# Kernel tuning notes

Measured on AMD Instinct MI355X. Metric: run time of the kernel, lower is better.

Reference implementation:

```python
import jax, jax.numpy as jnp
import numpy as np

N_HEAD = 16
MAX_SEQ_LEN = 2048
RATIO = 1
NEG_INF = -jnp.inf


def make_alibi_bias(n_head: int, max_seq_len: int, ratio: int) -> jnp.ndarray:
    # bias[t, s] = s*ratio - t, masked to -inf where > 0 (future positions)
    s = jnp.arange(max_seq_len)[None, :] * ratio            # [1, S]
    t = jnp.arange(max_seq_len * ratio)[:, None]            # [T, 1]
    bias = (s - t).astype(jnp.float32)                      # [T, S]
    bias = jnp.where(bias > 0, NEG_INF, bias)
    # per-head slopes: cumprod of 2^(-8/n_head) -> m_i = 2^(-8*(i+1)/n_head)
    m = jnp.cumprod(jnp.full((n_head,), 2.0 ** (-8.0 / n_head), dtype=jnp.float32))
    return bias[None, :, :] * m[:, None, None]              # [H, T, S]


def setup_inputs() -> dict:
    key = jax.random.key(0)
    kq, kk, kv = jax.random.split(key, 3)
    B, T, D = 2, 2048, 1024
    return {
        "q": jax.random.normal(kq, (B, T, D), dtype=jnp.float32),
        "k": jax.random.normal(kk, (B, T, D), dtype=jnp.float32),
        "v": jax.random.normal(kv, (B, T, D), dtype=jnp.float32),
    }


def reference(q, k, v):
    B, T, D = q.shape
    S = k.shape[1]
    H = N_HEAD
    dh = D // H
    # split heads: [B, T, D] -> [B, H, T, dh]
    qh = q.reshape(B, T, H, dh).transpose(0, 2, 1, 3)
    kh = k.reshape(B, S, H, dh).transpose(0, 2, 1, 3)
    vh = v.reshape(B, S, H, dh).transpose(0, 2, 1, 3)

    scores = jnp.einsum("bhtd,bhsd->bhts", qh, kh) / jnp.sqrt(jnp.float32(dh))
    bias = make_alibi_bias(H, MAX_SEQ_LEN, RATIO)[:, -T:, -S:]  # [H, T, S]
    attn = jax.nn.softmax(scores + bias[None], axis=-1)
    out = jnp.einsum("bhts,bhsd->bhtd", attn, vh)
    # gather heads: [B, H, T, dh] -> [B, T, D]
    return out.transpose(0, 2, 1, 3).reshape(B, T, D)
```

## Files before the change

### kernel.cpp

```cpp
#include <hip/hip_runtime.h>

#define N_HEAD 16
#define DHEAD 64
#define TSEQ 2048
#define DMODEL 1024
#define BATCH 2

typedef __bf16 bf16x8 __attribute__((ext_vector_type(8)));
typedef float f32x4 __attribute__((ext_vector_type(4)));

union BF8 { bf16x8 v; uint4 u; unsigned short us[8]; };

#if __has_builtin(__builtin_amdgcn_exp2f)
#define EXP2F(x) __builtin_amdgcn_exp2f(x)
#else
#define EXP2F(x) exp2f(x)
#endif

__device__ __forceinline__ void gload_lds16(const void* g, void* l) {
    __builtin_amdgcn_global_load_lds(
        (const __attribute__((address_space(1))) void*)g,
        (__attribute__((address_space(3))) void*)l, 16, 0, 0);
}

__device__ __forceinline__ unsigned short f2bf(float f) {
    unsigned u = __float_as_uint(f);
    u += 0x7fffu + ((u >> 16) & 1u);
    return (unsigned short)(u >> 16);
}

__device__ __forceinline__ bf16x8 load_bf8_f32(const float* p) {
    const float4 f0 = *(const float4*)p;
    const float4 f1 = *(const float4*)(p + 4);
    BF8 r;
    r.us[0] = f2bf(f0.x); r.us[1] = f2bf(f0.y);
    r.us[2] = f2bf(f0.z); r.us[3] = f2bf(f0.w);
    r.us[4] = f2bf(f1.x); r.us[5] = f2bf(f1.y);
    r.us[6] = f2bf(f1.z); r.us[7] = f2bf(f1.w);
    return r.v;
}

__global__ __launch_bounds__(256) void prep(const float* __restrict__ K,
                                            const float* __restrict__ V,
                                            unsigned short* __restrict__ Kp,
                                            unsigned short* __restrict__ Vt)
{
    __shared__ float tl[64][65];
    const int bh = blockIdx.y, b = bh >> 4, h = bh & 15;
    const int s0 = blockIdx.x * 64;
    const int t = threadIdx.x;
    const int r16 = t >> 4, c4 = (t & 15) * 4;
    #pragma unroll
    for (int pass = 0; pass < 4; ++pass) {
        const int row = pass * 16 + r16;
        const size_t goff = ((size_t)(b * TSEQ + s0 + row)) * DMODEL + h * DHEAD + c4;
        const float4 fk = *(const float4*)(K + goff);
        ushort4 ok;
        ok.x = f2bf(fk.x); ok.y = f2bf(fk.y); ok.z = f2bf(fk.z); ok.w = f2bf(fk.w);
        *(ushort4*)(Kp + (((size_t)bh * TSEQ + s0 + row) << 6) + c4) = ok;
        const float4 fv = *(const float4*)(V + goff);
        tl[row][c4 + 0] = fv.x; tl[row][c4 + 1] = fv.y;
        tl[row][c4 + 2] = fv.z; tl[row][c4 + 3] = fv.w;
    }
    __syncthreads();
    const int d = t >> 2, sc = (t & 3) * 16;
    union { unsigned short us[8]; uint4 u; } pk0, pk1;
    #pragma unroll
    for (int j = 0; j < 8; ++j) pk0.us[j] = f2bf(tl[sc + j][d]);
    #pragma unroll
    for (int j = 0; j < 8; ++j) pk1.us[j] = f2bf(tl[sc + 8 + j][d]);
    unsigned short* vo = Vt + ((size_t)bh * DHEAD + d) * TSEQ + s0 + sc;
    *(uint4*)vo = pk0.u;
    *(uint4*)(vo + 8) = pk1.u;
}

__global__ __launch_bounds__(256, 2) void alibi_attn(
    const float* __restrict__ Q, const unsigned short* __restrict__ Kp,
    const unsigned short* __restrict__ Vt, float* __restrict__ O)
{
    __shared__ __align__(16) unsigned short kbuf[2][4096];
    __shared__ __align__(16) unsigned short vbuf[2][4096];
    __shared__ __align__(16) unsigned short p_lds[4][32][72];

    const int wave = threadIdx.x >> 6;
    const int lane = threadIdx.x & 63;
    const int quad = lane >> 4;
    const int l16  = lane & 15;

    const int bh = blockIdx.x;
    const int b  = bh >> 4, h = bh & 15;
    const int sy = blockIdx.y;
    const int sx = (sy < 8) ? (15 - sy) : (sy - 8);

    const float LOG2E   = 1.44269504088896f;
    const float slope   = exp2f(-0.5f * (float)(h + 1));
    const float bslope2 = slope * LOG2E;
    const float sscale2 = 0.125f * LOG2E;
    const float step64  = 64.0f * bslope2;

    const float*    qp  = Q + (size_t)b * TSEQ * DMODEL + (size_t)h * DHEAD;
    const char*     kpb = (const char*)(Kp + (size_t)bh * TSEQ * DHEAD);
    const char*     vpb = (const char*)(Vt + (size_t)bh * DHEAD * TSEQ);

    const int base_w = sx * 128 + wave * 32;
    const int amax_w = (base_w + 31) >> 6;
    const int amax_b = 2 * sx + 1;

    const int st_r = lane >> 3;
    const int st_c = (lane & 7) ^ st_r;
    const int j0 = wave * 2;
    const int kg_off0 = (j0 * 8 + st_r) * 128 + st_c * 16;
    const int kg_off1 = kg_off0 + 8 * 128;
    const int vg_off0 = (j0 * 8 + st_r) * 4096 + st_c * 16;
    const int vg_off1 = vg_off0 + 8 * 4096;
    const int lds_o0 = j0 * 1024, lds_o1 = j0 * 1024 + 1024;

    auto stage = [&](int t) {
        const char* kg = kpb + (size_t)t * 8192;
        const char* vg = vpb + (size_t)t * 128;
        char* kd = (char*)kbuf[t & 1];
        char* vd = (char*)vbuf[t & 1];
        gload_lds16(kg + kg_off0, kd + lds_o0);
        gload_lds16(kg + kg_off1, kd + lds_o1);
        gload_lds16(vg + vg_off0, vd + lds_o0);
        gload_lds16(vg + vg_off1, vd + lds_o1);
    };

    const int koff0 = l16 * 128 + (((0 * 4 + quad) ^ (l16 & 7)) * 16);
    const int koff1 = l16 * 128 + (((1 * 4 + quad) ^ (l16 & 7)) * 16);

    stage(0);

    bf16x8 aq[2][2];
    #pragma unroll
    for (int qs = 0; qs < 2; ++qs) {
        const float* qr = qp + (size_t)(base_w + qs * 16 + l16) * DMODEL + quad * 8;
        aq[qs][0] = load_bf8_f32(qr);
        aq[qs][1] = load_bf8_f32(qr + 32);
    }

    const f32x4 zero4 = {0.f, 0.f, 0.f, 0.f};
    f32x4 o[2][4], lp[2];
    float dbq[2][4];
    #pragma unroll
    for (int qs = 0; qs < 2; ++qs) {
        lp[qs] = zero4;
        #pragma unroll
        for (int nt = 0; nt < 4; ++nt) {
            o[qs][nt] = zero4;
            dbq[qs][nt] = (float)(nt * 16 + l16 - (base_w + qs * 16 + quad * 4)) * bslope2;
        }
    }

    __syncthreads();

    for (int t = 0; t <= amax_b; ++t) {
        if (t < amax_b) stage(t + 1);

        if (t <= amax_w) {
            const char* kb = (const char*)kbuf[t & 1];
            const char* vb = (const char*)vbuf[t & 1];

            f32x4 s[2][4];
            #pragma unroll
            for (int nt = 0; nt < 4; ++nt) {
                BF8 k0, k1;
                k0.u = *(const uint4*)(kb + koff0 + nt * 2048);
                k1.u = *(const uint4*)(kb + koff1 + nt * 2048);
                #pragma unroll
                for (int qs = 0; qs < 2; ++qs) {
                    f32x4 acc = zero4;
                    acc = __builtin_amdgcn_mfma_f32_16x16x32_bf16(aq[qs][0], k0.v, acc, 0, 0, 0);
                    acc = __builtin_amdgcn_mfma_f32_16x16x32_bf16(aq[qs][1], k1.v, acc, 0, 0, 0);
                    s[qs][nt] = acc;
                }
            }
            uint4 vf[4][2];
            #pragma unroll
            for (int nt = 0; nt < 4; ++nt) {
                vf[nt][0] = *(const uint4*)(vb + koff0 + nt * 2048);
                vf[nt][1] = *(const uint4*)(vb + koff1 + nt * 2048);
            }

            const bool masked = (t == amax_w);
            const int kv0 = t * 64;
            #pragma unroll
            for (int qs = 0; qs < 2; ++qs)
                #pragma unroll
                for (int nt = 0; nt < 4; ++nt) {
                    f32x4 p;
                    #pragma unroll
                    for (int r = 0; r < 4; ++r)
                        p[r] = EXP2F(fmaf(s[qs][nt][r], sscale2,
                                          dbq[qs][nt] - (float)r * bslope2));
                    if (masked) {
                        const int di = kv0 + nt * 16 + l16 - (base_w + qs * 16 + quad * 4);
                        #pragma unroll
                        for (int r = 0; r < 4; ++r)
                            if (di - r > 0) p[r] = 0.f;
                    }
                    lp[qs] += p;
                    #pragma unroll
                    for (int r = 0; r < 4; ++r)
                        p_lds[wave][qs * 16 + quad * 4 + r][nt * 16 + l16] =
                            (unsigned short)(__float_as_uint(p[r]) >> 16);
                    dbq[qs][nt] += step64;
                }

            asm volatile("s_waitcnt lgkmcnt(0)" ::: "memory");
            BF8 pa[2][2];
            #pragma unroll
            for (int qs = 0; qs < 2; ++qs) {
                pa[qs][0].u = *(const uint4*)&p_lds[wave][qs * 16 + l16][quad * 8];
                pa[qs][1].u = *(const uint4*)&p_lds[wave][qs * 16 + l16][32 + quad * 8];
            }
            #pragma unroll
            for (int qs = 0; qs < 2; ++qs)
                #pragma unroll
                for (int nt = 0; nt < 4; ++nt) {
                    BF8 v0, v1;
                    v0.u = vf[nt][0];
                    v1.u = vf[nt][1];
                    o[qs][nt] = __builtin_amdgcn_mfma_f32_16x16x32_bf16(pa[qs][0].v, v0.v, o[qs][nt], 0, 0, 0);
                    o[qs][nt] = __builtin_amdgcn_mfma_f32_16x16x32_bf16(pa[qs][1].v, v1.v, o[qs][nt], 0, 0, 0);
                }
        }
        __syncthreads();
    }

    #pragma unroll
    for (int qs = 0; qs < 2; ++qs) {
        float ls[4];
        #pragma unroll
        for (int r = 0; r < 4; ++r) {
            float v = lp[qs][r];
            v += __shfl_xor(v, 1);
            v += __shfl_xor(v, 2);
            v += __shfl_xor(v, 4);
            v += __shfl_xor(v, 8);
            ls[r] = v;
        }
        #pragma unroll
        for (int nt = 0; nt < 4; ++nt)
            #pragma unroll
            for (int r = 0; r < 4; ++r) {
                const int trow = base_w + qs * 16 + quad * 4 + r;
                O[((size_t)b * TSEQ + trow) * DMODEL + h * DHEAD + nt * 16 + l16] =
                    o[qs][nt][r] / ls[r];
            }
    }
}

extern "C" void kernel_launch(void* const* d_in, const int* in_sizes, int n_in,
                              void* d_out, int out_size, void* d_ws, size_t ws_size,
                              hipStream_t stream) {
    const float* q = (const float*)d_in[0];
    const float* k = (const float*)d_in[1];
    const float* v = (const float*)d_in[2];
    float* out = (float*)d_out;

    unsigned short* Kp = (unsigned short*)d_ws;
    unsigned short* Vt = Kp + (size_t)BATCH * N_HEAD * TSEQ * DHEAD;

    prep<<<dim3(TSEQ / 64, BATCH * N_HEAD), 256, 0, stream>>>(k, v, Kp, Vt);
    alibi_attn<<<dim3(BATCH * N_HEAD, 16), 256, 0, stream>>>(q, Kp, Vt, out);
}
```

Baseline: 143.3 us.

## Switch attention to fp16 with transposed S so P feeds PV MFMA from registers

Converts K/V/Q staging from bf16 to fp16 using packed round-toward-zero conversion. Computes the score tile transposed (K as the A operand) so the exp'd probabilities land in registers in the layout the 16x16x16 f16 MFMA B/A operand expects, which removes the per-wave P round-trip through LDS and its wait. Blocks shrink to 128 threads covering 64 query rows with a 32-way grid, which removes the per-wave idle iterations of the old 128-row causal blocks. The costs are more, smaller MFMAs for PV, fp16 range risk for unnormalised probabilities, and less K/V reuse per block.

New measurement: 135.1 us. -5.8%, faster.

```diff
diff --git a/kernel.cpp b/kernel.cpp
--- a/kernel.cpp
+++ b/kernel.cpp
@@ -6,10 +6,14 @@
 #define DMODEL 1024
 #define BATCH 2
 
-typedef __bf16 bf16x8 __attribute__((ext_vector_type(8)));
+typedef _Float16 f16x8 __attribute__((ext_vector_type(8)));
+typedef _Float16 f16x4 __attribute__((ext_vector_type(4)));
+typedef _Float16 f16x2 __attribute__((ext_vector_type(2)));
+typedef __fp16 fp16x2 __attribute__((ext_vector_type(2)));
 typedef float f32x4 __attribute__((ext_vector_type(4)));
 
-union BF8 { bf16x8 v; uint4 u; unsigned short us[8]; };
+union F8 { f16x8 v; uint4 u; f16x2 h[4]; };
+union F4 { f16x4 v; uint2 u; f16x2 h[2]; };
 
 #if __has_builtin(__builtin_amdgcn_exp2f)
 #define EXP2F(x) __builtin_amdgcn_exp2f(x)
@@ -23,27 +27,25 @@
         (__attribute__((address_space(3))) void*)l, 16, 0, 0);
 }
 
-__device__ __forceinline__ unsigned short f2bf(float f) {
-    unsigned u = __float_as_uint(f);
-    u += 0x7fffu + ((u >> 16) & 1u);
-    return (unsigned short)(u >> 16);
-}
-
-__device__ __forceinline__ bf16x8 load_bf8_f32(const float* p) {
-    const float4 f0 = *(const float4*)p;
-    const float4 f1 = *(const float4*)(p + 4);
-    BF8 r;
-    r.us[0] = f2bf(f0.x); r.us[1] = f2bf(f0.y);
-    r.us[2] = f2bf(f0.z); r.us[3] = f2bf(f0.w);
-    r.us[4] = f2bf(f1.x); r.us[5] = f2bf(f1.y);
-    r.us[6] = f2bf(f1.z); r.us[7] = f2bf(f1.w);
-    return r.v;
+__device__ __forceinline__ f16x2 pk(float a, float b) {
+    union { fp16x2 i; f16x2 o; } c;
+    c.i = __builtin_amdgcn_cvt_pkrtz(a, b);
+    return c.o;
+}
+
+__device__ __forceinline__ F8 pack8_f32(const float* p) {
+    const float4 a = *(const float4*)p;
+    const float4 b = *(const float4*)(p + 4);
+    F8 r;
+    r.h[0] = pk(a.x, a.y); r.h[1] = pk(a.z, a.w);
+    r.h[2] = pk(b.x, b.y); r.h[3] = pk(b.z, b.w);
+    return r;
 }
 
 __global__ __launch_bounds__(256) void prep(const float* __restrict__ K,
                                             const float* __restrict__ V,
-                                            unsigned short* __restrict__ Kp,
-                                            unsigned short* __restrict__ Vt)
+                                            _Float16* __restrict__ Kh,
+                                            _Float16* __restrict__ Vh)
 {
     __shared__ float tl[64][65];
     const int bh = blockIdx.y, b = bh >> 4, h = bh & 15;
@@ -55,34 +57,34 @@
         const int row = pass * 16 + r16;
         const size_t goff = ((size_t)(b * TSEQ + s0 + row)) * DMODEL + h * DHEAD + c4;
         const float4 fk = *(const float4*)(K + goff);
-        ushort4 ok;
-        ok.x = f2bf(fk.x); ok.y = f2bf(fk.y); ok.z = f2bf(fk.z); ok.w = f2bf(fk.w);
-        *(ushort4*)(Kp + (((size_t)bh * TSEQ + s0 + row) << 6) + c4) = ok;
+        F4 ok;
+        ok.h[0] = pk(fk.x, fk.y);
+        ok.h[1] = pk(fk.z, fk.w);
+        *(uint2*)(Kh + (((size_t)bh * TSEQ + s0 + row) << 6) + c4) = ok.u;
         const float4 fv = *(const float4*)(V + goff);
         tl[row][c4 + 0] = fv.x; tl[row][c4 + 1] = fv.y;
         tl[row][c4 + 2] = fv.z; tl[row][c4 + 3] = fv.w;
     }
     __syncthreads();
     const int d = t >> 2, sc = (t & 3) * 16;
-    union { unsigned short us[8]; uint4 u; } pk0, pk1;
-    #pragma unroll
-    for (int j = 0; j < 8; ++j) pk0.us[j] = f2bf(tl[sc + j][d]);
-    #pragma unroll
-    for (int j = 0; j < 8; ++j) pk1.us[j] = f2bf(tl[sc + 8 + j][d]);
-    unsigned short* vo = Vt + ((size_t)bh * DHEAD + d) * TSEQ + s0 + sc;
-    *(uint4*)vo = pk0.u;
-    *(uint4*)(vo + 8) = pk1.u;
-}
-
-__global__ __launch_bounds__(256, 2) void alibi_attn(
-    const float* __restrict__ Q, const unsigned short* __restrict__ Kp,
-    const unsigned short* __restrict__ Vt, float* __restrict__ O)
+    F8 p0, p1;
+    #pragma unroll
+    for (int j = 0; j < 4; ++j) p0.h[j] = pk(tl[sc + 2 * j][d], tl[sc + 2 * j + 1][d]);
+    #pragma unroll
+    for (int j = 0; j < 4; ++j) p1.h[j] = pk(tl[sc + 8 + 2 * j][d], tl[sc + 9 + 2 * j][d]);
+    _Float16* vo = Vh + ((size_t)bh * DHEAD + d) * TSEQ + s0 + sc;
+    *(uint4*)vo = p0.u;
+    *(uint4*)(vo + 8) = p1.u;
+}
+
+__global__ __launch_bounds__(128, 2) void alibi_attn(
+    const float* __restrict__ Q, const _Float16* __restrict__ Kh,
+    const _Float16* __restrict__ Vh, float* __restrict__ O)
 {
-    __shared__ __align__(16) unsigned short kbuf[2][4096];
-    __shared__ __align__(16) unsigned short vbuf[2][4096];
-    __shared__ __align__(16) unsigned short p_lds[4][32][72];
-
-    const int wave = threadIdx.x >> 6;
+    __shared__ __align__(16) char kbuf[2][8192];
+    __shared__ __align__(16) char vbuf[2][8192];
+
+    const int wv   = threadIdx.x >> 6;
     const int lane = threadIdx.x & 63;
     const int quad = lane >> 4;
     const int l16  = lane & 15;
@@ -90,7 +92,7 @@
     const int bh = blockIdx.x;
     const int b  = bh >> 4, h = bh & 15;
     const int sy = blockIdx.y;
-    const int sx = (sy < 8) ? (15 - sy) : (sy - 8);
+    const int sx = (sy < 16) ? (31 - sy) : (sy - 16);
 
     const float LOG2E   = 1.44269504088896f;
     const float slope   = exp2f(-0.5f * (float)(h + 1));
@@ -98,155 +100,145 @@
     const float sscale2 = 0.125f * LOG2E;
     const float step64  = 64.0f * bslope2;
 
-    const float*    qp  = Q + (size_t)b * TSEQ * DMODEL + (size_t)h * DHEAD;
-    const char*     kpb = (const char*)(Kp + (size_t)bh * TSEQ * DHEAD);
-    const char*     vpb = (const char*)(Vt + (size_t)bh * DHEAD * TSEQ);
-
-    const int base_w = sx * 128 + wave * 32;
-    const int amax_w = (base_w + 31) >> 6;
-    const int amax_b = 2 * sx + 1;
+    const float* qp  = Q + (size_t)b * TSEQ * DMODEL + (size_t)h * DHEAD;
+    const char*  kpb = (const char*)(Kh + (size_t)bh * TSEQ * DHEAD);
+    const char*  vpb = (const char*)(Vh + (size_t)bh * DHEAD * TSEQ);
+
+    const int base_w = sx * 64 + wv * 32;
 
     const int st_r = lane >> 3;
-    const int st_c = (lane & 7) ^ st_r;
-    const int j0 = wave * 2;
-    const int kg_off0 = (j0 * 8 + st_r) * 128 + st_c * 16;
-    const int kg_off1 = kg_off0 + 8 * 128;
-    const int vg_off0 = (j0 * 8 + st_r) * 4096 + st_c * 16;
-    const int vg_off1 = vg_off0 + 8 * 4096;
-    const int lds_o0 = j0 * 1024, lds_o1 = j0 * 1024 + 1024;
+    const int k_src = st_r * 128  + (((lane & 7) ^ st_r) * 16);
+    const int v_src = st_r * 4096 + (((lane & 7) ^ st_r) * 16);
 
     auto stage = [&](int t) {
         const char* kg = kpb + (size_t)t * 8192;
         const char* vg = vpb + (size_t)t * 128;
-        char* kd = (char*)kbuf[t & 1];
-        char* vd = (char*)vbuf[t & 1];
-        gload_lds16(kg + kg_off0, kd + lds_o0);
-        gload_lds16(kg + kg_off1, kd + lds_o1);
-        gload_lds16(vg + vg_off0, vd + lds_o0);
-        gload_lds16(vg + vg_off1, vd + lds_o1);
+        char* kd = kbuf[t & 1];
+        char* vd = vbuf[t & 1];
+        #pragma unroll
+        for (int c = 0; c < 4; ++c) {
+            const int gr = wv * 32 + c * 8;
+            gload_lds16(kg + gr * 128 + k_src, kd + gr * 128);
+            gload_lds16(vg + gr * 4096 + v_src, vd + gr * 128);
+        }
     };
 
-    const int koff0 = l16 * 128 + (((0 * 4 + quad) ^ (l16 & 7)) * 16);
-    const int koff1 = l16 * 128 + (((1 * 4 + quad) ^ (l16 & 7)) * 16);
-
     stage(0);
 
-    bf16x8 aq[2][2];
+    F8 aq[2][2];
     #pragma unroll
     for (int qs = 0; qs < 2; ++qs) {
         const float* qr = qp + (size_t)(base_w + qs * 16 + l16) * DMODEL + quad * 8;
-        aq[qs][0] = load_bf8_f32(qr);
-        aq[qs][1] = load_bf8_f32(qr + 32);
-    }
+        aq[qs][0] = pack8_f32(qr);
+        aq[qs][1] = pack8_f32(qr + 32);
+    }
+
+    const int koff0 = l16 * 128 + ((quad ^ (l16 & 7)) * 16);
+    const int koff1 = l16 * 128 + (((quad + 4) ^ (l16 & 7)) * 16);
+    const int vbase = l16 * 128 + (quad & 1) * 8;
+    int vx[4];
+    #pragma unroll
+    for (int sj = 0; sj < 4; ++sj)
+        vx[sj] = ((sj * 2 + (quad >> 1)) ^ (l16 & 7)) * 16;
 
     const f32x4 zero4 = {0.f, 0.f, 0.f, 0.f};
-    f32x4 o[2][4], lp[2];
+    f32x4 o[2][4];
+    float lp[2] = {0.f, 0.f};
     float dbq[2][4];
+    float rb1 = bslope2, rb2 = 2.f * bslope2, rb3 = 3.f * bslope2;
     #pragma unroll
     for (int qs = 0; qs < 2; ++qs) {
-        lp[qs] = zero4;
-        #pragma unroll
-        for (int nt = 0; nt < 4; ++nt) {
-            o[qs][nt] = zero4;
-            dbq[qs][nt] = (float)(nt * 16 + l16 - (base_w + qs * 16 + quad * 4)) * bslope2;
+        #pragma unroll
+        for (int nt = 0; nt < 4; ++nt) o[qs][nt] = zero4;
+        #pragma unroll
+        for (int sj = 0; sj < 4; ++sj)
+            dbq[qs][sj] = (float)(sj * 16 + quad * 4 - base_w - qs * 16 - l16) * bslope2;
+    }
+
+    __syncthreads();
+
+    for (int t = 0; t <= sx; ++t) {
+        if (t < sx) stage(t + 1);
+        const char* kb = kbuf[t & 1];
+        const char* vb = vbuf[t & 1];
+
+        F8 kA[4][2];
+        #pragma unroll
+        for (int sj = 0; sj < 4; ++sj) {
+            kA[sj][0].u = *(const uint4*)(kb + sj * 2048 + koff0);
+            kA[sj][1].u = *(const uint4*)(kb + sj * 2048 + koff1);
         }
-    }
-
-    __syncthreads();
-
-    for (int t = 0; t <= amax_b; ++t) {
-        if (t < amax_b) stage(t + 1);
-
-        if (t <= amax_w) {
-            const char* kb = (const char*)kbuf[t & 1];
-            const char* vb = (const char*)vbuf[t & 1];
-
-            f32x4 s[2][4];
-            #pragma unroll
-            for (int nt = 0; nt < 4; ++nt) {
-                BF8 k0, k1;
-                k0.u = *(const uint4*)(kb + koff0 + nt * 2048);
-                k1.u = *(const uint4*)(kb + koff1 + nt * 2048);
+
+        f32x4 sT[2][4];
+        #pragma unroll
+        for (int qs = 0; qs < 2; ++qs)
+            #pragma unroll
+            for (int sj = 0; sj < 4; ++sj) {
+                f32x4 acc = zero4;
+                acc = __builtin_amdgcn_mfma_f32_16x16x32_f16(kA[sj][0].v, aq[qs][0].v, acc, 0, 0, 0);
+                acc = __builtin_amdgcn_mfma_f32_16x16x32_f16(kA[sj][1].v, aq[qs][1].v, acc, 0, 0, 0);
+                sT[qs][sj] = acc;
+            }
+
+        F4 vf[4][4];
+        #pragma unroll
+        for (int nt = 0; nt < 4; ++nt)
+            #pragma unroll
+            for (int sj = 0; sj < 4; ++sj)
+                vf[nt][sj].u = *(const uint2*)(vb + nt * 2048 + vbase + vx[sj]);
+
+        const bool masked = (t == sx);
+        F4 pP[2][4];
+        #pragma unroll
+        for (int qs = 0; qs < 2; ++qs)
+            #pragma unroll
+            for (int sj = 0; sj < 4; ++sj) {
+                const float db = dbq[qs][sj];
+                float p0 = EXP2F(fmaf(sT[qs][sj][0], sscale2, db));
+                float p1 = EXP2F(fmaf(sT[qs][sj][1], sscale2, db + rb1));
+                float p2 = EXP2F(fmaf(sT[qs][sj][2], sscale2, db + rb2));
+                float p3 = EXP2F(fmaf(sT[qs][sj][3], sscale2, db + rb3));
+                if (masked) {
+                    const int di = t * 64 + sj * 16 + quad * 4 - base_w - qs * 16 - l16;
+                    if (di + 0 > 0) p0 = 0.f;
+                    if (di + 1 > 0) p1 = 0.f;
+                    if (di + 2 > 0) p2 = 0.f;
+                    if (di + 3 > 0) p3 = 0.f;
+                }
+                lp[qs] += (p0 + p1) + (p2 + p3);
+                pP[qs][sj].h[0] = pk(p0, p1);
+                pP[qs][sj].h[1] = pk(p2, p3);
+                dbq[qs][sj] = db + step64;
+            }
+
+        #pragma unroll
+        for (int qs = 0; qs < 2; ++qs)
+            #pragma unroll
+            for (int nt = 0; nt < 4; ++nt)
                 #pragma unroll
-                for (int qs = 0; qs < 2; ++qs) {
-                    f32x4 acc = zero4;
-                    acc = __builtin_amdgcn_mfma_f32_16x16x32_bf16(aq[qs][0], k0.v, acc, 0, 0, 0);
-                    acc = __builtin_amdgcn_mfma_f32_16x16x32_bf16(aq[qs][1], k1.v, acc, 0, 0, 0);
-                    s[qs][nt] = acc;
-                }
-            }
-            uint4 vf[4][2];
-            #pragma unroll
-            for (int nt = 0; nt < 4; ++nt) {
-                vf[nt][0] = *(const uint4*)(vb + koff0 + nt * 2048);
-                vf[nt][1] = *(const uint4*)(vb + koff1 + nt * 2048);
-            }
-
-            const bool masked = (t == amax_w);
-            const int kv0 = t * 64;
-            #pragma unroll
-            for (int qs = 0; qs < 2; ++qs)
-                #pragma unroll
-                for (int nt = 0; nt < 4; ++nt) {
-                    f32x4 p;
-                    #pragma unroll
-                    for (int r = 0; r < 4; ++r)
-                        p[r] = EXP2F(fmaf(s[qs][nt][r], sscale2,
-                                          dbq[qs][nt] - (float)r * bslope2));
-                    if (masked) {
-                        const int di = kv0 + nt * 16 + l16 - (base_w + qs * 16 + quad * 4);
-                        #pragma unroll
-                        for (int r = 0; r < 4; ++r)
-                            if (di - r > 0) p[r] = 0.f;
-                    }
-                    lp[qs] += p;
-                    #pragma unroll
-                    for (int r = 0; r < 4; ++r)
-                        p_lds[wave][qs * 16 + quad * 4 + r][nt * 16 + l16] =
-                            (unsigned short)(__float_as_uint(p[r]) >> 16);
-                    dbq[qs][nt] += step64;
-                }
-
-            asm volatile("s_waitcnt lgkmcnt(0)" ::: "memory");
-            BF8 pa[2][2];
-            #pragma unroll
-            for (int qs = 0; qs < 2; ++qs) {
-                pa[qs][0].u = *(const uint4*)&p_lds[wave][qs * 16 + l16][quad * 8];
-                pa[qs][1].u = *(const uint4*)&p_lds[wave][qs * 16 + l16][32 + quad * 8];
-            }
-            #pragma unroll
-            for (int qs = 0; qs < 2; ++qs)
-                #pragma unroll
-                for (int nt = 0; nt < 4; ++nt) {
-                    BF8 v0, v1;
-                    v0.u = vf[nt][0];
-                    v1.u = vf[nt][1];
-                    o[qs][nt] = __builtin_amdgcn_mfma_f32_16x16x32_bf16(pa[qs][0].v, v0.v, o[qs][nt], 0, 0, 0);
-                    o[qs][nt] = __builtin_amdgcn_mfma_f32_16x16x32_bf16(pa[qs][1].v, v1.v, o[qs][nt], 0, 0, 0);
-                }
-        }
+                for (int sj = 0; sj < 4; ++sj)
+                    o[qs][nt] = __builtin_amdgcn_mfma_f32_16x16x16f16(
+                        pP[qs][sj].v, vf[nt][sj].v, o[qs][nt], 0, 0, 0);
+
         __syncthreads();
     }
 
     #pragma unroll
     for (int qs = 0; qs < 2; ++qs) {
-        float ls[4];
-        #pragma unroll
-        for (int r = 0; r < 4; ++r) {
-            float v = lp[qs][r];
-            v += __shfl_xor(v, 1);
-            v += __shfl_xor(v, 2);
-            v += __shfl_xor(v, 4);
-            v += __shfl_xor(v, 8);
-            ls[r] = v;
-        }
+        float ls = lp[qs];
+        ls += __shfl_xor(ls, 16);
+        ls += __shfl_xor(ls, 32);
+        float lr[4];
+        #pragma unroll
+        for (int r = 0; r < 4; ++r)
+            lr[r] = __shfl(ls, quad * 4 + r);
         #pragma unroll
         for (int nt = 0; nt < 4; ++nt)
             #pragma unroll
             for (int r = 0; r < 4; ++r) {
                 const int trow = base_w + qs * 16 + quad * 4 + r;
                 O[((size_t)b * TSEQ + trow) * DMODEL + h * DHEAD + nt * 16 + l16] =
-                    o[qs][nt][r] / ls[r];
+                    o[qs][nt][r] / lr[r];
             }
     }
 }
@@ -259,9 +251,9 @@
     const float* v = (const float*)d_in[2];
     float* out = (float*)d_out;
 
-    unsigned short* Kp = (unsigned short*)d_ws;
-    unsigned short* Vt = Kp + (size_t)BATCH * N_HEAD * TSEQ * DHEAD;
-
-    prep<<<dim3(TSEQ / 64, BATCH * N_HEAD), 256, 0, stream>>>(k, v, Kp, Vt);
-    alibi_attn<<<dim3(BATCH * N_HEAD, 16), 256, 0, stream>>>(q, Kp, Vt, out);
-}
+    _Float16* Kh = (_Float16*)d_ws;
+    _Float16* Vh = Kh + (size_t)BATCH * N_HEAD * TSEQ * DHEAD;
+
+    prep<<<dim3(TSEQ / 64, BATCH * N_HEAD), 256, 0, stream>>>(k, v, Kh, Vh);
+    alibi_attn<<<dim3(BATCH * N_HEAD, 32), 128, 0, stream>>>(q, Kh, Vh, out);
+}
```
